# Performance work log

Measured on AMD Instinct MI355X. Metric: run time of the kernel, lower is better.

The kernel has to match this reference:

```python
import jax, jax.numpy as jnp
import numpy as np

H, HD = 8, 64  # num_heads, head_dim
EPS = 1e-6

def rmsnorm(x, scale):
    return x * jax.lax.rsqrt(jnp.mean(x * x, axis=-1, keepdims=True) + EPS) * scale

def lecun(key, shape):
    fan_in = shape[0]
    return jax.random.normal(key, shape, dtype=jnp.float32) * (fan_in ** -0.5)

def setup_inputs() -> dict:
    key = jax.random.key(0)
    ks = jax.random.split(key, 12)
    B, S, D = 2, 512, 512
    hidden = H * HD            # 512
    ffn = 4 * D                # 2048
    return {
        "inputs": jax.random.normal(ks[0], (B, S, D), dtype=jnp.float32),
        "mask": jnp.zeros((B, S), dtype=jnp.float32),
        "carry": jnp.zeros((B, H, HD, HD), dtype=jnp.float32),
        "ln1": jnp.ones((D,), dtype=jnp.float32),
        "Wq": lecun(ks[1], (D, hidden)),
        "Wk": lecun(ks[2], (D, hidden)),
        "Wv": lecun(ks[3], (D, hidden)),
        "attn_ln": jnp.ones((hidden,), dtype=jnp.float32),
        "Wo": lecun(ks[4], (hidden, D)),
        "bo": jnp.zeros((D,), dtype=jnp.float32),
        "ln2": jnp.ones((D,), dtype=jnp.float32),
        "Wg": lecun(ks[5], (D, ffn)),
        "Wu": lecun(ks[6], (D, ffn)),
        "Wd": lecun(ks[7], (ffn, D)),
    }

def reference(inputs, mask, carry, ln1, Wq, Wk, Wv, attn_ln, Wo, bo, ln2, Wg, Wu, Wd):
    B, S, D = inputs.shape
    skip = inputs
    x = rmsnorm(inputs, ln1)
    # projections + relu feature map
    q = jax.nn.relu((x @ Wq).reshape(B, S, H, HD))
    k = jax.nn.relu((x @ Wk).reshape(B, S, H, HD))
    v = (x @ Wv).reshape(B, S, H, HD)
    # matrix-valued state update: Bmat_t = v_t k_t^T  [B,S,H,HD,HD]
    Bmat = v[..., :, None] * k[..., None, :]
    # decay: identity, zeroed where mask==1 (episode reset)
    m = mask[:, :, None, None, None]
    A = jnp.broadcast_to(jnp.eye(HD, dtype=x.dtype), Bmat.shape) * (1.0 - m)

    def binop(lhs, rhs):
        a_i, b_i = lhs
        a_j, b_j = rhs
        return jnp.matmul(a_i, a_j), jnp.matmul(b_i, a_j) + b_j

    cum_decay, hidden_states = jax.lax.associative_scan(binop, (A, Bmat), axis=1)
    # fold in incoming carry
    states = jnp.matmul(carry[:, None], cum_decay) + hidden_states  # [B,S,H,HD,HD]
    attn = jnp.matmul(states, q[..., None]).squeeze(-1).reshape(B, S, H * HD)
    attn = rmsnorm(attn, attn_ln)
    y = attn @ Wo + bo
    final_carry = states[:, -1]
    # residual + SwiGLU FFN
    x = y + skip
    skip2 = x
    x = rmsnorm(x, ln2)
    x = (jax.nn.silu(x @ Wg) * (x @ Wu)) @ Wd
    return (final_carry, x + skip2)
```

## Files before the change

kernel.cpp:

```cpp
#include <hip/hip_runtime.h>
#include <math.h>

typedef __bf16 bf16x8 __attribute__((ext_vector_type(8)));
typedef float  f32x4  __attribute__((ext_vector_type(4)));

constexpr int B_=2, S_=512, D_=512, H_=8, HD_=64, FFN_=2048, NC_=8;
constexpr float EPS_=1e-6f;

__device__ __forceinline__ __bf16 f2bf(float f){
    union{float f;unsigned u;}x; x.f=f;
    unsigned r=(x.u+0x7fffu+((x.u>>16)&1u))>>16;
    union{unsigned short s;__bf16 b;}y; y.s=(unsigned short)r; return y.b;
}
__device__ __forceinline__ float bf2f(unsigned short s){
    union{unsigned u;float f;}x; x.u=((unsigned)s)<<16; return x.f;
}
__device__ __forceinline__ void bf8_f32(uint4 p, float* o){
    unsigned w[4]={p.x,p.y,p.z,p.w};
#pragma unroll
    for(int i=0;i<4;i++){ o[2*i]=bf2f((unsigned short)(w[i]&0xffffu)); o[2*i+1]=bf2f((unsigned short)(w[i]>>16)); }
}
__device__ __forceinline__ f32x4 MF(bf16x8 a, bf16x8 b, f32x4 c){
    return __builtin_amdgcn_mfma_f32_16x16x32_bf16(a,b,c,0,0,0);
}
#define GLOAD16(g,l) __builtin_amdgcn_global_load_lds((__attribute__((address_space(1))) const void*)(g),(__attribute__((address_space(3))) void*)(l),16,0,0)

__device__ __forceinline__ void rowsq_atomic(float* accb, int row0, int lane, float p[4]){
#pragma unroll
    for(int r=0;r<4;r++){
        float v = p[r];
        v += __shfl_xor(v, 1, 64);
        v += __shfl_xor(v, 2, 64);
        v += __shfl_xor(v, 4, 64);
        v += __shfl_xor(v, 8, 64);
        if((lane&15)==0) atomicAdd(accb + row0 + r, v);
    }
}

__global__ __launch_bounds__(256) void prep_k(const float* __restrict__ Wg,
    const float* __restrict__ Wu, const float* __restrict__ Wd,
    const float* __restrict__ Wq, const float* __restrict__ Wk,
    const float* __restrict__ Wv, const float* __restrict__ Wo,
    __bf16* __restrict__ WT, const float* __restrict__ inputs,
    float* __restrict__ rs1, float* __restrict__ rs2acc, float* __restrict__ rs3acc){
    __shared__ __bf16 s[64][72];
    int t = blockIdx.x, tid = threadIdx.x;
    if(t >= 1024){
        int row = (t-1024)*4 + (tid>>6), lane = tid&63;
        const float4* p = (const float4*)(inputs + (size_t)row*D_) + lane*2;
        float4 a=p[0], b=p[1];
        float ss = a.x*a.x+a.y*a.y+a.z*a.z+a.w*a.w + b.x*b.x+b.y*b.y+b.z*b.z+b.w*b.w;
        for(int off=32; off>0; off>>=1) ss += __shfl_down(ss, off, 64);
        if(lane==0) rs1[row] = rsqrtf(ss/(float)D_ + EPS_);
        float4 z = {0.f,0.f,0.f,0.f};
        if(t==1024) ((float4*)rs2acc)[tid] = z;
        if(t==1025) ((float4*)rs3acc)[tid] = z;
        return;
    }
    const float* src; __bf16* dst; int K,N,lt;
    if      (t<256){ src=Wg; dst=WT;          K=512;  N=2048; lt=t; }
    else if (t<512){ src=Wu; dst=WT+1048576;  K=512;  N=2048; lt=t-256; }
    else if (t<768){ src=Wd; dst=WT+2097152;  K=2048; N=512;  lt=t-512; }
    else if (t<832){ src=Wq; dst=WT+3145728;  K=512;  N=512;  lt=t-768; }
    else if (t<896){ src=Wk; dst=WT+3407872;  K=512;  N=512;  lt=t-832; }
    else if (t<960){ src=Wv; dst=WT+3670016;  K=512;  N=512;  lt=t-896; }
    else           { src=Wo; dst=WT+3932160;  K=512;  N=512;  lt=t-960; }
    int nt64 = N>>6, tk = lt/nt64, tn = lt%nt64;
    {
        int jk = tid>>2, jn0 = (tid&3)*16;
        const float* p = src + (size_t)(tk*64+jk)*N + tn*64 + jn0;
        float4 a0=((const float4*)p)[0], a1=((const float4*)p)[1],
               a2=((const float4*)p)[2], a3=((const float4*)p)[3];
        bf16x8 w0, w1;
        w0[0]=f2bf(a0.x); w0[1]=f2bf(a0.y); w0[2]=f2bf(a0.z); w0[3]=f2bf(a0.w);
        w0[4]=f2bf(a1.x); w0[5]=f2bf(a1.y); w0[6]=f2bf(a1.z); w0[7]=f2bf(a1.w);
        w1[0]=f2bf(a2.x); w1[1]=f2bf(a2.y); w1[2]=f2bf(a2.z); w1[3]=f2bf(a2.w);
        w1[4]=f2bf(a3.x); w1[5]=f2bf(a3.y); w1[6]=f2bf(a3.z); w1[7]=f2bf(a3.w);
        *(bf16x8*)&s[jk][jn0] = w0; *(bf16x8*)&s[jk][jn0+8] = w1;
    }
    __syncthreads();
    {
        int jn = tid>>2, jk0 = (tid&3)*16;
        bf16x8 w0, w1;
#pragma unroll
        for(int j=0;j<8;j++){ w0[j]=s[jk0+j][jn]; w1[j]=s[jk0+8+j][jn]; }
        __bf16* q = dst + (size_t)(tn*64+jn)*K + tk*64 + jk0;
        *(bf16x8*)q = w0; *(bf16x8*)(q+8) = w1;
    }
}

__device__ __forceinline__ void stageB2(const __bf16* __restrict__ Bt, int n0, int K, int kk,
                                        __bf16* sB0, __bf16* sB1, int wave, int lane){
    int row = (wave<<4) + (lane>>2), kq = (lane&3)<<3;
    const __bf16* g = Bt + (size_t)(n0+row)*K + kk + kq;
    GLOAD16(g,      sB0 + (wave<<9));
    GLOAD16(g + 32, sB1 + (wave<<9));
    const __bf16* g2 = g + (size_t)64*K;
    GLOAD16(g2,      sB0 + 2048 + (wave<<9));
    GLOAD16(g2 + 32, sB1 + 2048 + (wave<<9));
}
__device__ __forceinline__ void stageB1(const __bf16* __restrict__ Bt, int n0, int K, int kk,
                                        __bf16* sB0, __bf16* sB1, int wave, int lane){
    int row = (wave<<4) + (lane>>2), kq = (lane&3)<<3;
    const __bf16* g = Bt + (size_t)(n0+row)*K + kk + kq;
    GLOAD16(g,      sB0 + (wave<<9));
    GLOAD16(g + 32, sB1 + (wave<<9));
}
__device__ __forceinline__ void stageA_rms_f32(const float* __restrict__ A, const float* __restrict__ rs,
        const float* __restrict__ g, int m0, int K, int kk, __bf16* sA0, __bf16* sA1, int tid){
    int row = tid>>2, kq = (tid&3)<<4;
    float r = rs[m0+row];
    const float4* p = (const float4*)(A + (size_t)(m0+row)*K + kk + kq);
    const float4* gp = (const float4*)(g + kk + kq);
    float4 a[4] = {p[0],p[1],p[2],p[3]};
    float4 gg[4] = {gp[0],gp[1],gp[2],gp[3]};
    bf16x8 w0, w1;
    w0[0]=f2bf(a[0].x*r*gg[0].x); w0[1]=f2bf(a[0].y*r*gg[0].y);
    w0[2]=f2bf(a[0].z*r*gg[0].z); w0[3]=f2bf(a[0].w*r*gg[0].w);
    w0[4]=f2bf(a[1].x*r*gg[1].x); w0[5]=f2bf(a[1].y*r*gg[1].y);
    w0[6]=f2bf(a[1].z*r*gg[1].z); w0[7]=f2bf(a[1].w*r*gg[1].w);
    w1[0]=f2bf(a[2].x*r*gg[2].x); w1[1]=f2bf(a[2].y*r*gg[2].y);
    w1[2]=f2bf(a[2].z*r*gg[2].z); w1[3]=f2bf(a[2].w*r*gg[2].w);
    w1[4]=f2bf(a[3].x*r*gg[3].x); w1[5]=f2bf(a[3].y*r*gg[3].y);
    w1[6]=f2bf(a[3].z*r*gg[3].z); w1[7]=f2bf(a[3].w*r*gg[3].w);
    __bf16* d = (kq<32) ? (sA0 + row*32 + kq) : (sA1 + row*32 + kq-32);
    *(bf16x8*)d = w0; *(bf16x8*)(d+8) = w1;
}
__device__ __forceinline__ void stageA_rms_acc(const __bf16* __restrict__ A, const float* __restrict__ ssq,
        const float* __restrict__ g, int m0, int K, int kk, __bf16* sA0, __bf16* sA1, int tid){
    int row = tid>>2, kq = (tid&3)<<4;
    float r = rsqrtf(ssq[m0+row]*(1.f/(float)D_) + EPS_);
    const __bf16* p = A + (size_t)(m0+row)*K + kk + kq;
    float v[16]; bf8_f32(*(const uint4*)p, v); bf8_f32(*(const uint4*)(p+8), v+8);
    const float4* gp = (const float4*)(g + kk + kq);
    float4 gg[4] = {gp[0],gp[1],gp[2],gp[3]};
    float gf[16] = {gg[0].x,gg[0].y,gg[0].z,gg[0].w, gg[1].x,gg[1].y,gg[1].z,gg[1].w,
                    gg[2].x,gg[2].y,gg[2].z,gg[2].w, gg[3].x,gg[3].y,gg[3].z,gg[3].w};
    bf16x8 w0, w1;
#pragma unroll
    for(int j=0;j<8;j++){ w0[j]=f2bf(v[j]*r*gf[j]); w1[j]=f2bf(v[8+j]*r*gf[8+j]); }
    __bf16* d = (kq<32) ? (sA0 + row*32 + kq) : (sA1 + row*32 + kq-32);
    *(bf16x8*)d = w0; *(bf16x8*)(d+8) = w1;
}
__device__ __forceinline__ void mfma_tile(const __bf16* sA0, const __bf16* sA1,
        const __bf16* sB0, const __bf16* sB1, int wave, int lane, f32x4 acc[4]){
    int ar = (((wave<<4)+(lane&15))<<5) + ((lane>>4)<<3);
    bf16x8 a0 = *(const bf16x8*)(sA0+ar);
    bf16x8 a1 = *(const bf16x8*)(sA1+ar);
#pragma unroll
    for(int nt=0;nt<4;nt++){
        int br = (((nt<<4)+(lane&15))<<5) + ((lane>>4)<<3);
        acc[nt] = MF(a0, *(const bf16x8*)(sB0+br), acc[nt]);
        acc[nt] = MF(a1, *(const bf16x8*)(sB1+br), acc[nt]);
    }
}
__device__ __forceinline__ void mfma_tile8(const __bf16* sA0, const __bf16* sA1,
        const __bf16* sB0, const __bf16* sB1, int wave, int lane, f32x4 acc[8]){
    int ar = (((wave<<4)+(lane&15))<<5) + ((lane>>4)<<3);
    bf16x8 a0 = *(const bf16x8*)(sA0+ar);
    bf16x8 a1 = *(const bf16x8*)(sA1+ar);
#pragma unroll
    for(int nt=0;nt<8;nt++){
        int br = (((nt<<4)+(lane&15))<<5) + ((lane>>4)<<3);
        acc[nt] = MF(a0, *(const bf16x8*)(sB0+br), acc[nt]);
        acc[nt] = MF(a1, *(const bf16x8*)(sB1+br), acc[nt]);
    }
}

__global__ __launch_bounds__(256) void gemm_qkv_k(const float* __restrict__ in,
        const float* __restrict__ rs1, const float* __restrict__ ln1,
        const __bf16* __restrict__ Bt, __bf16* __restrict__ Qb,
        __bf16* __restrict__ Kb, __bf16* __restrict__ Vb){
    __shared__ __bf16 sA0[2048], sA1[2048], sB0[4096], sB1[4096];
    int tid=threadIdx.x, wave=tid>>6, lane=tid&63;
    int n0 = blockIdx.x*128, m0 = blockIdx.y*64;
    f32x4 acc[8] = {};
    for(int kk=0; kk<512; kk+=64){
        stageB2(Bt, n0, 512, kk, sB0, sB1, wave, lane);
        stageA_rms_f32(in, rs1, ln1, m0, 512, kk, sA0, sA1, tid);
        __syncthreads();
        mfma_tile8(sA0,sA1,sB0,sB1,wave,lane,acc);
        __syncthreads();
    }
    int seg = n0>>9, nc = n0&511;
    __bf16* Out = seg==0 ? Qb : (seg==1 ? Kb : Vb);
    bool rl = seg<2;
    int r0 = (wave<<4) + ((lane>>4)<<2);
#pragma unroll
    for(int nt=0;nt<8;nt++){
        int col = nc + nt*16 + (lane&15);
#pragma unroll
        for(int r=0;r<4;r++){
            float v = acc[nt][r]; if(rl) v = fmaxf(v,0.f);
            Out[(size_t)(m0+r0+r)*512 + col] = f2bf(v);
        }
    }
}

__global__ __launch_bounds__(256) void scanA_k(const __bf16* __restrict__ Kb,
        const __bf16* __restrict__ Vb, const float* __restrict__ mask,
        __bf16* __restrict__ MS, float* __restrict__ Pws){
    int bid = blockIdx.x;
    int c = bid&7, h = (bid>>3)&7, b = bid>>6;
    __shared__ __bf16 sKT0[2048], sKT1[2048], sVT0[2048], sVT1[2048];
    __shared__ float scv[64], ssp[64];
    int tid = threadIdx.x, wave = tid>>6, lane = tid&63;
    const __bf16* Kg = Kb + (size_t)(b*512 + c*64)*512 + h*64;
    const __bf16* Vg = Vb + (size_t)(b*512 + c*64)*512 + h*64;
    if(tid<64) scv[tid] = 1.f - mask[b*512 + c*64 + tid];
    __syncthreads();
    if(tid==0){
        float sp = 1.f;
        for(int t=63;t>=0;--t){ ssp[t]=sp; sp*=scv[t]; }
        Pws[bid] = sp;
    }
    __syncthreads();
#pragma unroll
    for(int p=0;p<2;p++){
        int t = (tid>>3) + p*32, i0 = (tid&7)*8;
        uint4 kr = *(const uint4*)(Kg + (size_t)t*512 + i0);
        uint4 vr = *(const uint4*)(Vg + (size_t)t*512 + i0);
        const __bf16* kp = (const __bf16*)&kr;
        const unsigned short* vp = (const unsigned short*)&vr;
        float sp = ssp[t];
        __bf16* kh = p ? sKT1 : sKT0;
        __bf16* vh = p ? sVT1 : sVT0;
#pragma unroll
        for(int j=0;j<8;j++){
            kh[(i0+j)*32 + (t&31)] = kp[j];
            vh[(i0+j)*32 + (t&31)] = f2bf(bf2f(vp[j])*sp);
        }
    }
    __syncthreads();
    f32x4 am[4] = {};
    mfma_tile(sVT0, sVT1, sKT0, sKT1, wave, lane, am);
    __bf16* Mo = MS + (size_t)bid*4096;
    int r0 = (wave<<4) + ((lane>>4)<<2);
#pragma unroll
    for(int nt=0;nt<4;nt++){
        int j = nt*16 + (lane&15);
#pragma unroll
        for(int r=0;r<4;r++) Mo[(size_t)(r0+r)*64 + j] = f2bf(am[nt][r]);
    }
}

__global__ __launch_bounds__(256) void scanC_k(const __bf16* __restrict__ Qb,
        const __bf16* __restrict__ Kb, const __bf16* __restrict__ Vb,
        const float* __restrict__ mask, const __bf16* __restrict__ MS,
        const float* __restrict__ carry, const float* __restrict__ Pws,
        float* __restrict__ carry_out, __bf16* __restrict__ attn,
        float* __restrict__ rs2acc){
    int bid = blockIdx.x;
    int c = bid&7, h = (bid>>3)&7, b = bid>>6;
    int bh = b*H_ + h;
    __shared__ __bf16 sQ0[2048], sQ1[2048], sK0[2048], sK1[2048];
    __shared__ __bf16 sS0[2048], sS1[2048];
    __shared__ __bf16 sVT0[2048], sVT1[2048];
    __shared__ __bf16 sW0[2048], sW1[2048];
    __shared__ float Wtab[64][64];
    __shared__ float scv[64], pp[64];
    int tid = threadIdx.x, wave = tid>>6, lane = tid&63;
    const __bf16* Qg = Qb + (size_t)(b*512 + c*64)*512 + h*64;
    const __bf16* Kg = Kb + (size_t)(b*512 + c*64)*512 + h*64;
    const __bf16* Vg = Vb + (size_t)(b*512 + c*64)*512 + h*64;

    stageB1(Qg, 0, 512, 0, sQ0, sQ1, wave, lane);
    stageB1(Kg, 0, 512, 0, sK0, sK1, wave, lane);
    if(tid<64) scv[tid] = 1.f - mask[b*512 + c*64 + tid];
#pragma unroll
    for(int p=0;p<2;p++){
        int u = (tid>>3) + p*32, i0 = (tid&7)*8;
        uint4 vr = *(const uint4*)(Vg + (size_t)u*512 + i0);
        const __bf16* vp = (const __bf16*)&vr;
        __bf16* vh = p ? sVT1 : sVT0;
#pragma unroll
        for(int j=0;j<8;j++) vh[(i0+j)*32 + (u&31)] = vp[j];
    }
    {
        int i = tid>>2, j0 = (tid&3)*16;
        float s[16];
        const float* ci = carry + (size_t)bh*4096 + i*64 + j0;
        const float4* c4 = (const float4*)ci;
        float4 s4[4] = {c4[0],c4[1],c4[2],c4[3]};
        float* sp = (float*)s4;
#pragma unroll
        for(int j=0;j<16;j++) s[j]=sp[j];
        for(int cc=0; cc<c; ++cc){
            float P = Pws[bh*8+cc];
            const __bf16* mp = MS + ((size_t)bh*8+cc)*4096 + i*64 + j0;
            float mv[16]; bf8_f32(*(const uint4*)mp, mv); bf8_f32(*(const uint4*)(mp+8), mv+8);
#pragma unroll
            for(int j=0;j<16;j++) s[j] = s[j]*P + mv[j];
        }
        bf16x8 w0, w1;
#pragma unroll
        for(int j=0;j<8;j++){ w0[j]=f2bf(s[j]); w1[j]=f2bf(s[8+j]); }
        __bf16* d = (j0<32) ? (sS0 + i*32 + j0) : (sS1 + i*32 + j0-32);
        *(bf16x8*)d = w0; *(bf16x8*)(d+8) = w1;
        if(c==7){
            float P = Pws[bh*8+7];
            const __bf16* mp = MS + ((size_t)bh*8+7)*4096 + i*64 + j0;
            float mv[16]; bf8_f32(*(const uint4*)mp, mv); bf8_f32(*(const uint4*)(mp+8), mv+8);
            float4 o4[4];
            float* ov = (float*)o4;
#pragma unroll
            for(int j=0;j<16;j++) ov[j] = s[j]*P + mv[j];
            float4* co = (float4*)(carry_out + (size_t)bh*4096 + i*64 + j0);
            co[0]=o4[0]; co[1]=o4[1]; co[2]=o4[2]; co[3]=o4[3];
        }
    }
    __syncthreads();
    if(tid<64){
        int u = tid; float w = 1.f;
        for(int t=0;t<64;t++){
            if(t>u) w *= scv[t];
            Wtab[u][t] = (t<u) ? 0.f : w;
        }
    }
    if(tid==64){
        float p=1.f;
        for(int t=0;t<64;t++){ p*=scv[t]; pp[t]=p; }
    }
    f32x4 sc[4] = {};
    mfma_tile(sK0, sK1, sQ0, sQ1, wave, lane, sc);
    __syncthreads();
    {
        int u0 = (wave<<4) + ((lane>>4)<<2);
#pragma unroll
        for(int nt=0;nt<4;nt++){
            int t = nt*16 + (lane&15);
#pragma unroll
            for(int r=0;r<4;r++){
                int u = u0 + r;
                float v = sc[nt][r] * Wtab[u][t];
                ((u<32) ? sW0 : sW1)[t*32 + (u&31)] = f2bf(v);
            }
        }
    }
    __syncthreads();
    f32x4 aI[4] = {}, aX[4] = {};
    mfma_tile(sW0, sW1, sVT0, sVT1, wave, lane, aI);
    mfma_tile(sQ0, sQ1, sS0, sS1, wave, lane, aX);
    int t0 = (wave<<4) + ((lane>>4)<<2);
    float psum[4] = {0.f,0.f,0.f,0.f};
#pragma unroll
    for(int nt=0;nt<4;nt++){
        int i = nt*16 + (lane&15);
#pragma unroll
        for(int r=0;r<4;r++){
            int t = t0 + r;
            float o = aI[nt][r] + aX[nt][r]*pp[t];
            attn[(size_t)(b*512 + c*64 + t)*512 + h*64 + i] = f2bf(o);
            psum[r] += o*o;
        }
    }
    rowsq_atomic(rs2acc, b*512 + c*64 + t0, lane, psum);
}

__global__ __launch_bounds__(256) void gemm_wo_k(const __bf16* __restrict__ attn,
        const float* __restrict__ rs2acc, const float* __restrict__ aln,
        const __bf16* __restrict__ Bt, const float* __restrict__ bo,
        const float* __restrict__ skip, float* __restrict__ outx,
        __bf16* __restrict__ X1, float* __restrict__ rs3acc){
    __shared__ __bf16 sA0[2048], sA1[2048], sB0[4096], sB1[4096];
    int tid=threadIdx.x, wave=tid>>6, lane=tid&63;
    int n0 = blockIdx.x*128, m0 = blockIdx.y*64;
    f32x4 acc[8] = {};
    for(int kk=0; kk<512; kk+=64){
        stageB2(Bt, n0, 512, kk, sB0, sB1, wave, lane);
        stageA_rms_acc(attn, rs2acc, aln, m0, 512, kk, sA0, sA1, tid);
        __syncthreads();
        mfma_tile8(sA0,sA1,sB0,sB1,wave,lane,acc);
        __syncthreads();
    }
    int r0 = (wave<<4) + ((lane>>4)<<2);
    float psum[4] = {0.f,0.f,0.f,0.f};
#pragma unroll
    for(int nt=0;nt<8;nt++){
        int col = n0 + nt*16 + (lane&15);
#pragma unroll
        for(int r=0;r<4;r++){
            int row = m0+r0+r;
            float v = acc[nt][r] + bo[col] + skip[(size_t)row*512+col];
            outx[(size_t)row*512+col] = v;
            X1[(size_t)row*512+col] = f2bf(v);
            psum[r] += v*v;
        }
    }
    rowsq_atomic(rs3acc, m0+r0, lane, psum);
}

__global__ __launch_bounds__(256) void gemm_dual_k(const __bf16* __restrict__ X1,
        const float* __restrict__ rs3acc, const float* __restrict__ ln2,
        const __bf16* __restrict__ Gt, const __bf16* __restrict__ Ut,
        __bf16* __restrict__ Hb){
    __shared__ __bf16 sA0[2048], sA1[2048], sG0[4096], sG1[4096], sU0[4096], sU1[4096];
    int tid=threadIdx.x, wave=tid>>6, lane=tid&63;
    int n0 = blockIdx.x*128, m0 = blockIdx.y*64;
    f32x4 ag[8] = {}, au[8] = {};
    for(int kk=0; kk<512; kk+=64){
        stageB2(Gt, n0, 512, kk, sG0, sG1, wave, lane);
        stageB2(Ut, n0, 512, kk, sU0, sU1, wave, lane);
        stageA_rms_acc(X1, rs3acc, ln2, m0, 512, kk, sA0, sA1, tid);
        __syncthreads();
        {
            int ar = (((wave<<4)+(lane&15))<<5) + ((lane>>4)<<3);
            bf16x8 a0 = *(const bf16x8*)(sA0+ar);
            bf16x8 a1 = *(const bf16x8*)(sA1+ar);
#pragma unroll
            for(int nt=0;nt<8;nt++){
                int br = (((nt<<4)+(lane&15))<<5) + ((lane>>4)<<3);
                ag[nt] = MF(a0, *(const bf16x8*)(sG0+br), ag[nt]);
                ag[nt] = MF(a1, *(const bf16x8*)(sG1+br), ag[nt]);
                au[nt] = MF(a0, *(const bf16x8*)(sU0+br), au[nt]);
                au[nt] = MF(a1, *(const bf16x8*)(sU1+br), au[nt]);
            }
        }
        __syncthreads();
    }
    int r0 = (wave<<4) + ((lane>>4)<<2);
#pragma unroll
    for(int nt=0;nt<8;nt++){
        int col = n0 + nt*16 + (lane&15);
#pragma unroll
        for(int r=0;r<4;r++){
            float gv = ag[nt][r], uv = au[nt][r];
            float hv = (gv / (1.f + __expf(-gv))) * uv;
            Hb[(size_t)(m0+r0+r)*FFN_ + col] = f2bf(hv);
        }
    }
}

__global__ __launch_bounds__(256) void gemm_wd_k(const __bf16* __restrict__ Hb,
        const __bf16* __restrict__ Bt, float* __restrict__ outx){
    __shared__ __bf16 sA0[2048], sA1[2048], sB0[4096], sB1[4096];
    int tid=threadIdx.x, wave=tid>>6, lane=tid&63;
    int n0 = blockIdx.x*128, m0 = blockIdx.y*64, ks = blockIdx.z*512;
    f32x4 acc[8] = {};
    int row = (wave<<4) + (lane>>2), kq = (lane&3)<<3;
    for(int kk=ks; kk<ks+512; kk+=64){
        stageB2(Bt, n0, FFN_, kk, sB0, sB1, wave, lane);
        const __bf16* g = Hb + (size_t)(m0+row)*FFN_ + kk + kq;
        GLOAD16(g,      sA0 + (wave<<9));
        GLOAD16(g + 32, sA1 + (wave<<9));
        __syncthreads();
        mfma_tile8(sA0,sA1,sB0,sB1,wave,lane,acc);
        __syncthreads();
    }
    int r0 = (wave<<4) + ((lane>>4)<<2);
#pragma unroll
    for(int nt=0;nt<8;nt++){
        int col = n0 + nt*16 + (lane&15);
#pragma unroll
        for(int r=0;r<4;r++)
            atomicAdd(&outx[(size_t)(m0+r0+r)*512 + col], acc[nt][r]);
    }
}

extern "C" void kernel_launch(void* const* d_in, const int* in_sizes, int n_in,
                              void* d_out, int out_size, void* d_ws, size_t ws_size,
                              hipStream_t stream) {
    const float* inputs  = (const float*)d_in[0];
    const float* mask    = (const float*)d_in[1];
    const float* carry   = (const float*)d_in[2];
    const float* ln1     = (const float*)d_in[3];
    const float* Wq      = (const float*)d_in[4];
    const float* Wk      = (const float*)d_in[5];
    const float* Wv      = (const float*)d_in[6];
    const float* attn_ln = (const float*)d_in[7];
    const float* Wo      = (const float*)d_in[8];
    const float* bo      = (const float*)d_in[9];
    const float* ln2     = (const float*)d_in[10];
    const float* Wg      = (const float*)d_in[11];
    const float* Wu      = (const float*)d_in[12];
    const float* Wd      = (const float*)d_in[13];

    float* out_carry = (float*)d_out;
    float* out_x     = (float*)d_out + 65536;

    __bf16* wb = (__bf16*)d_ws;
    float*  wf = (float*)d_ws;
    __bf16* WgT   = wb;
    __bf16* WuT   = wb + 1048576;
    __bf16* WdT   = wb + 2097152;
    __bf16* WqkvT = wb + 3145728;
    __bf16* WoT   = wb + 3932160;
    __bf16* Qb    = wb + 4194304;
    __bf16* Kb    = wb + 4718592;
    __bf16* Vb    = wb + 5242880;
    __bf16* Hb    = wb + 3145728;
    __bf16* MS    = wb + 5767168;
    float*  Pws   = wf + 3145728;
    float*  rs1   = wf + 3145856;
    float*  rs2a  = wf + 3146880;
    float*  rs3a  = wf + 3147904;

    prep_k<<<dim3(1280), dim3(256), 0, stream>>>(Wg,Wu,Wd,Wq,Wk,Wv,Wo, wb, inputs, rs1, rs2a, rs3a);
    gemm_qkv_k<<<dim3(12,16), dim3(256), 0, stream>>>(inputs, rs1, ln1, WqkvT, Qb, Kb, Vb);
    scanA_k<<<dim3(128), dim3(256), 0, stream>>>(Kb, Vb, mask, MS, Pws);
    scanC_k<<<dim3(128), dim3(256), 0, stream>>>(Qb, Kb, Vb, mask, MS, carry, Pws, out_carry, Qb, rs2a);
    gemm_wo_k<<<dim3(4,16), dim3(256), 0, stream>>>(Qb, rs2a, attn_ln, WoT, bo, inputs, out_x, Vb, rs3a);
    gemm_dual_k<<<dim3(16,16), dim3(256), 0, stream>>>(Vb, rs3a, ln2, WgT, WuT, Hb);
    gemm_wd_k<<<dim3(4,16,4), dim3(256), 0, stream>>>(Hb, WdT, out_x);
}
```

Measured before the change: 169.9 us.

## Double-buffer GEMM shared tiles and halve N-tile to raise block count

All four GEMM kernels (qkv, wo, dual gate/up, wd) switch to double-buffered LDS. The next K-slice's global loads are issued before the MFMA on the current slice, and one barrier per iteration replaces two. The N tile shrinks from 128 to 64, so the grids double and more workgroups run on the many CUs. The RMS scale is now loaded once per kernel instead of per K-step, and the prep transpose's read mapping is changed to reduce LDS bank conflicts. Smaller tiles mean less B-reuse and more A reloads.

```diff
diff --git a/kernel.cpp b/kernel.cpp
--- a/kernel.cpp
+++ b/kernel.cpp
@@ -80,25 +80,15 @@
     }
     __syncthreads();
     {
-        int jn = tid>>2, jk0 = (tid&3)*16;
+        int jn = tid&63, jkq = (tid>>6)*16;
         bf16x8 w0, w1;
 #pragma unroll
-        for(int j=0;j<8;j++){ w0[j]=s[jk0+j][jn]; w1[j]=s[jk0+8+j][jn]; }
-        __bf16* q = dst + (size_t)(tn*64+jn)*K + tk*64 + jk0;
+        for(int j=0;j<8;j++){ w0[j]=s[jkq+j][jn]; w1[j]=s[jkq+8+j][jn]; }
+        __bf16* q = dst + (size_t)(tn*64+jn)*K + tk*64 + jkq;
         *(bf16x8*)q = w0; *(bf16x8*)(q+8) = w1;
     }
 }
 
-__device__ __forceinline__ void stageB2(const __bf16* __restrict__ Bt, int n0, int K, int kk,
-                                        __bf16* sB0, __bf16* sB1, int wave, int lane){
-    int row = (wave<<4) + (lane>>2), kq = (lane&3)<<3;
-    const __bf16* g = Bt + (size_t)(n0+row)*K + kk + kq;
-    GLOAD16(g,      sB0 + (wave<<9));
-    GLOAD16(g + 32, sB1 + (wave<<9));
-    const __bf16* g2 = g + (size_t)64*K;
-    GLOAD16(g2,      sB0 + 2048 + (wave<<9));
-    GLOAD16(g2 + 32, sB1 + 2048 + (wave<<9));
-}
 __device__ __forceinline__ void stageB1(const __bf16* __restrict__ Bt, int n0, int K, int kk,
                                         __bf16* sB0, __bf16* sB1, int wave, int lane){
     int row = (wave<<4) + (lane>>2), kq = (lane&3)<<3;
@@ -106,36 +96,47 @@
     GLOAD16(g,      sB0 + (wave<<9));
     GLOAD16(g + 32, sB1 + (wave<<9));
 }
-__device__ __forceinline__ void stageA_rms_f32(const float* __restrict__ A, const float* __restrict__ rs,
-        const float* __restrict__ g, int m0, int K, int kk, __bf16* sA0, __bf16* sA1, int tid){
+struct ARf { float4 a0,a1,a2,a3, g0,g1,g2,g3; };
+__device__ __forceinline__ ARf loadA_f32(const float* __restrict__ A, const float* __restrict__ g,
+                                         int m0, int K, int kk, int tid){
     int row = tid>>2, kq = (tid&3)<<4;
-    float r = rs[m0+row];
     const float4* p = (const float4*)(A + (size_t)(m0+row)*K + kk + kq);
     const float4* gp = (const float4*)(g + kk + kq);
-    float4 a[4] = {p[0],p[1],p[2],p[3]};
-    float4 gg[4] = {gp[0],gp[1],gp[2],gp[3]};
+    ARf o;
+    o.a0=p[0]; o.a1=p[1]; o.a2=p[2]; o.a3=p[3];
+    o.g0=gp[0]; o.g1=gp[1]; o.g2=gp[2]; o.g3=gp[3];
+    return o;
+}
+__device__ __forceinline__ void writeA_f32(const ARf& o, float r, __bf16* sA0, __bf16* sA1, int tid){
+    int row = tid>>2, kq = (tid&3)<<4;
     bf16x8 w0, w1;
-    w0[0]=f2bf(a[0].x*r*gg[0].x); w0[1]=f2bf(a[0].y*r*gg[0].y);
-    w0[2]=f2bf(a[0].z*r*gg[0].z); w0[3]=f2bf(a[0].w*r*gg[0].w);
-    w0[4]=f2bf(a[1].x*r*gg[1].x); w0[5]=f2bf(a[1].y*r*gg[1].y);
-    w0[6]=f2bf(a[1].z*r*gg[1].z); w0[7]=f2bf(a[1].w*r*gg[1].w);
-    w1[0]=f2bf(a[2].x*r*gg[2].x); w1[1]=f2bf(a[2].y*r*gg[2].y);
-    w1[2]=f2bf(a[2].z*r*gg[2].z); w1[3]=f2bf(a[2].w*r*gg[2].w);
-    w1[4]=f2bf(a[3].x*r*gg[3].x); w1[5]=f2bf(a[3].y*r*gg[3].y);
-    w1[6]=f2bf(a[3].z*r*gg[3].z); w1[7]=f2bf(a[3].w*r*gg[3].w);
+    w0[0]=f2bf(o.a0.x*r*o.g0.x); w0[1]=f2bf(o.a0.y*r*o.g0.y);
+    w0[2]=f2bf(o.a0.z*r*o.g0.z); w0[3]=f2bf(o.a0.w*r*o.g0.w);
+    w0[4]=f2bf(o.a1.x*r*o.g1.x); w0[5]=f2bf(o.a1.y*r*o.g1.y);
+    w0[6]=f2bf(o.a1.z*r*o.g1.z); w0[7]=f2bf(o.a1.w*r*o.g1.w);
+    w1[0]=f2bf(o.a2.x*r*o.g2.x); w1[1]=f2bf(o.a2.y*r*o.g2.y);
+    w1[2]=f2bf(o.a2.z*r*o.g2.z); w1[3]=f2bf(o.a2.w*r*o.g2.w);
+    w1[4]=f2bf(o.a3.x*r*o.g3.x); w1[5]=f2bf(o.a3.y*r*o.g3.y);
+    w1[6]=f2bf(o.a3.z*r*o.g3.z); w1[7]=f2bf(o.a3.w*r*o.g3.w);
     __bf16* d = (kq<32) ? (sA0 + row*32 + kq) : (sA1 + row*32 + kq-32);
     *(bf16x8*)d = w0; *(bf16x8*)(d+8) = w1;
 }
-__device__ __forceinline__ void stageA_rms_acc(const __bf16* __restrict__ A, const float* __restrict__ ssq,
-        const float* __restrict__ g, int m0, int K, int kk, __bf16* sA0, __bf16* sA1, int tid){
+struct ARb { uint4 p0,p1; float4 g0,g1,g2,g3; };
+__device__ __forceinline__ ARb loadA_bf16(const __bf16* __restrict__ A, const float* __restrict__ g,
+                                          int m0, int K, int kk, int tid){
     int row = tid>>2, kq = (tid&3)<<4;
-    float r = rsqrtf(ssq[m0+row]*(1.f/(float)D_) + EPS_);
     const __bf16* p = A + (size_t)(m0+row)*K + kk + kq;
-    float v[16]; bf8_f32(*(const uint4*)p, v); bf8_f32(*(const uint4*)(p+8), v+8);
     const float4* gp = (const float4*)(g + kk + kq);
-    float4 gg[4] = {gp[0],gp[1],gp[2],gp[3]};
-    float gf[16] = {gg[0].x,gg[0].y,gg[0].z,gg[0].w, gg[1].x,gg[1].y,gg[1].z,gg[1].w,
-                    gg[2].x,gg[2].y,gg[2].z,gg[2].w, gg[3].x,gg[3].y,gg[3].z,gg[3].w};
+    ARb o;
+    o.p0 = *(const uint4*)p; o.p1 = *(const uint4*)(p+8);
+    o.g0=gp[0]; o.g1=gp[1]; o.g2=gp[2]; o.g3=gp[3];
+    return o;
+}
+__device__ __forceinline__ void writeA_bf16(const ARb& o, float r, __bf16* sA0, __bf16* sA1, int tid){
+    int row = tid>>2, kq = (tid&3)<<4;
+    float v[16]; bf8_f32(o.p0, v); bf8_f32(o.p1, v+8);
+    float gf[16] = {o.g0.x,o.g0.y,o.g0.z,o.g0.w, o.g1.x,o.g1.y,o.g1.z,o.g1.w,
+                    o.g2.x,o.g2.y,o.g2.z,o.g2.w, o.g3.x,o.g3.y,o.g3.z,o.g3.w};
     bf16x8 w0, w1;
 #pragma unroll
     for(int j=0;j<8;j++){ w0[j]=f2bf(v[j]*r*gf[j]); w1[j]=f2bf(v[8+j]*r*gf[8+j]); }
@@ -154,45 +155,47 @@
         acc[nt] = MF(a1, *(const bf16x8*)(sB1+br), acc[nt]);
     }
 }
-__device__ __forceinline__ void mfma_tile8(const __bf16* sA0, const __bf16* sA1,
-        const __bf16* sB0, const __bf16* sB1, int wave, int lane, f32x4 acc[8]){
-    int ar = (((wave<<4)+(lane&15))<<5) + ((lane>>4)<<3);
-    bf16x8 a0 = *(const bf16x8*)(sA0+ar);
-    bf16x8 a1 = *(const bf16x8*)(sA1+ar);
-#pragma unroll
-    for(int nt=0;nt<8;nt++){
-        int br = (((nt<<4)+(lane&15))<<5) + ((lane>>4)<<3);
-        acc[nt] = MF(a0, *(const bf16x8*)(sB0+br), acc[nt]);
-        acc[nt] = MF(a1, *(const bf16x8*)(sB1+br), acc[nt]);
-    }
-}
 
 __global__ __launch_bounds__(256) void gemm_qkv_k(const float* __restrict__ in,
         const float* __restrict__ rs1, const float* __restrict__ ln1,
         const __bf16* __restrict__ Bt, __bf16* __restrict__ Qb,
         __bf16* __restrict__ Kb, __bf16* __restrict__ Vb){
-    __shared__ __bf16 sA0[2048], sA1[2048], sB0[4096], sB1[4096];
+    __shared__ __bf16 sA0[2][2048], sA1[2][2048], sB0[2][2048], sB1[2][2048];
     int tid=threadIdx.x, wave=tid>>6, lane=tid&63;
-    int n0 = blockIdx.x*128, m0 = blockIdx.y*64;
-    f32x4 acc[8] = {};
-    for(int kk=0; kk<512; kk+=64){
-        stageB2(Bt, n0, 512, kk, sB0, sB1, wave, lane);
-        stageA_rms_f32(in, rs1, ln1, m0, 512, kk, sA0, sA1, tid);
-        __syncthreads();
-        mfma_tile8(sA0,sA1,sB0,sB1,wave,lane,acc);
-        __syncthreads();
+    int n0 = blockIdx.x*64, m0 = blockIdx.y*64;
+    float r = rs1[m0+(tid>>2)];
+    f32x4 acc[4] = {};
+    {
+        ARf a = loadA_f32(in, ln1, m0, 512, 0, tid);
+        stageB1(Bt, n0, 512, 0, sB0[0], sB1[0], wave, lane);
+        writeA_f32(a, r, sA0[0], sA1[0], tid);
+        __syncthreads();
+    }
+    int cur = 0;
+#pragma unroll
+    for(int it=0; it<8; ++it){
+        int nxt = cur^1;
+        ARf a;
+        if(it<7){
+            a = loadA_f32(in, ln1, m0, 512, (it+1)*64, tid);
+            stageB1(Bt, n0, 512, (it+1)*64, sB0[nxt], sB1[nxt], wave, lane);
+        }
+        mfma_tile(sA0[cur],sA1[cur],sB0[cur],sB1[cur],wave,lane,acc);
+        if(it<7) writeA_f32(a, r, sA0[nxt], sA1[nxt], tid);
+        __syncthreads();
+        cur = nxt;
     }
     int seg = n0>>9, nc = n0&511;
     __bf16* Out = seg==0 ? Qb : (seg==1 ? Kb : Vb);
     bool rl = seg<2;
     int r0 = (wave<<4) + ((lane>>4)<<2);
 #pragma unroll
-    for(int nt=0;nt<8;nt++){
+    for(int nt=0;nt<4;nt++){
         int col = nc + nt*16 + (lane&15);
 #pragma unroll
-        for(int r=0;r<4;r++){
-            float v = acc[nt][r]; if(rl) v = fmaxf(v,0.f);
-            Out[(size_t)(m0+r0+r)*512 + col] = f2bf(v);
+        for(int rr=0;rr<4;rr++){
+            float v = acc[nt][rr]; if(rl) v = fmaxf(v,0.f);
+            Out[(size_t)(m0+r0+rr)*512 + col] = f2bf(v);
         }
     }
 }
@@ -279,8 +282,7 @@
     {
         int i = tid>>2, j0 = (tid&3)*16;
         float s[16];
-        const float* ci = carry + (size_t)bh*4096 + i*64 + j0;
-        const float4* c4 = (const float4*)ci;
+        const float4* c4 = (const float4*)(carry + (size_t)bh*4096 + i*64 + j0);
         float4 s4[4] = {c4[0],c4[1],c4[2],c4[3]};
         float* sp = (float*)s4;
 #pragma unroll
@@ -362,29 +364,43 @@
         const __bf16* __restrict__ Bt, const float* __restrict__ bo,
         const float* __restrict__ skip, float* __restrict__ outx,
         __bf16* __restrict__ X1, float* __restrict__ rs3acc){
-    __shared__ __bf16 sA0[2048], sA1[2048], sB0[4096], sB1[4096];
+    __shared__ __bf16 sA0[2][2048], sA1[2][2048], sB0[2][2048], sB1[2][2048];
     int tid=threadIdx.x, wave=tid>>6, lane=tid&63;
-    int n0 = blockIdx.x*128, m0 = blockIdx.y*64;
-    f32x4 acc[8] = {};
-    for(int kk=0; kk<512; kk+=64){
-        stageB2(Bt, n0, 512, kk, sB0, sB1, wave, lane);
-        stageA_rms_acc(attn, rs2acc, aln, m0, 512, kk, sA0, sA1, tid);
-        __syncthreads();
-        mfma_tile8(sA0,sA1,sB0,sB1,wave,lane,acc);
-        __syncthreads();
+    int n0 = blockIdx.x*64, m0 = blockIdx.y*64;
+    float r = rsqrtf(rs2acc[m0+(tid>>2)]*(1.f/(float)D_) + EPS_);
+    f32x4 acc[4] = {};
+    {
+        ARb a = loadA_bf16(attn, aln, m0, 512, 0, tid);
+        stageB1(Bt, n0, 512, 0, sB0[0], sB1[0], wave, lane);
+        writeA_bf16(a, r, sA0[0], sA1[0], tid);
+        __syncthreads();
+    }
+    int cur = 0;
+#pragma unroll
+    for(int it=0; it<8; ++it){
+        int nxt = cur^1;
+        ARb a;
+        if(it<7){
+            a = loadA_bf16(attn, aln, m0, 512, (it+1)*64, tid);
+            stageB1(Bt, n0, 512, (it+1)*64, sB0[nxt], sB1[nxt], wave, lane);
+        }
+        mfma_tile(sA0[cur],sA1[cur],sB0[cur],sB1[cur],wave,lane,acc);
+        if(it<7) writeA_bf16(a, r, sA0[nxt], sA1[nxt], tid);
+        __syncthreads();
+        cur = nxt;
     }
     int r0 = (wave<<4) + ((lane>>4)<<2);
     float psum[4] = {0.f,0.f,0.f,0.f};
 #pragma unroll
-    for(int nt=0;nt<8;nt++){
+    for(int nt=0;nt<4;nt++){
         int col = n0 + nt*16 + (lane&15);
 #pragma unroll
-        for(int r=0;r<4;r++){
-            int row = m0+r0+r;
-            float v = acc[nt][r] + bo[col] + skip[(size_t)row*512+col];
+        for(int rr=0;rr<4;rr++){
+            int row = m0+r0+rr;
+            float v = acc[nt][rr] + bo[col] + skip[(size_t)row*512+col];
             outx[(size_t)row*512+col] = v;
             X1[(size_t)row*512+col] = f2bf(v);
-            psum[r] += v*v;
+            psum[rr] += v*v;
         }
     }
     rowsq_atomic(rs3acc, m0+r0, lane, psum);
@@ -394,62 +410,91 @@
         const float* __restrict__ rs3acc, const float* __restrict__ ln2,
         const __bf16* __restrict__ Gt, const __bf16* __restrict__ Ut,
         __bf16* __restrict__ Hb){
-    __shared__ __bf16 sA0[2048], sA1[2048], sG0[4096], sG1[4096], sU0[4096], sU1[4096];
+    __shared__ __bf16 sA0[2][2048], sA1[2][2048];
+    __shared__ __bf16 sG0[2][2048], sG1[2][2048], sU0[2][2048], sU1[2][2048];
     int tid=threadIdx.x, wave=tid>>6, lane=tid&63;
-    int n0 = blockIdx.x*128, m0 = blockIdx.y*64;
-    f32x4 ag[8] = {}, au[8] = {};
-    for(int kk=0; kk<512; kk+=64){
-        stageB2(Gt, n0, 512, kk, sG0, sG1, wave, lane);
-        stageB2(Ut, n0, 512, kk, sU0, sU1, wave, lane);
-        stageA_rms_acc(X1, rs3acc, ln2, m0, 512, kk, sA0, sA1, tid);
-        __syncthreads();
+    int n0 = blockIdx.x*64, m0 = blockIdx.y*64;
+    float r = rsqrtf(rs3acc[m0+(tid>>2)]*(1.f/(float)D_) + EPS_);
+    f32x4 ag[4] = {}, au[4] = {};
+    {
+        ARb a = loadA_bf16(X1, ln2, m0, 512, 0, tid);
+        stageB1(Gt, n0, 512, 0, sG0[0], sG1[0], wave, lane);
+        stageB1(Ut, n0, 512, 0, sU0[0], sU1[0], wave, lane);
+        writeA_bf16(a, r, sA0[0], sA1[0], tid);
+        __syncthreads();
+    }
+    int cur = 0;
+#pragma unroll
+    for(int it=0; it<8; ++it){
+        int nxt = cur^1;
+        ARb a;
+        if(it<7){
+            a = loadA_bf16(X1, ln2, m0, 512, (it+1)*64, tid);
+            stageB1(Gt, n0, 512, (it+1)*64, sG0[nxt], sG1[nxt], wave, lane);
+            stageB1(Ut, n0, 512, (it+1)*64, sU0[nxt], sU1[nxt], wave, lane);
+        }
         {
             int ar = (((wave<<4)+(lane&15))<<5) + ((lane>>4)<<3);
-            bf16x8 a0 = *(const bf16x8*)(sA0+ar);
-            bf16x8 a1 = *(const bf16x8*)(sA1+ar);
-#pragma unroll
-            for(int nt=0;nt<8;nt++){
+            bf16x8 a0 = *(const bf16x8*)(sA0[cur]+ar);
+            bf16x8 a1 = *(const bf16x8*)(sA1[cur]+ar);
+#pragma unroll
+            for(int nt=0;nt<4;nt++){
                 int br = (((nt<<4)+(lane&15))<<5) + ((lane>>4)<<3);
-                ag[nt] = MF(a0, *(const bf16x8*)(sG0+br), ag[nt]);
-                ag[nt] = MF(a1, *(const bf16x8*)(sG1+br), ag[nt]);
-                au[nt] = MF(a0, *(const bf16x8*)(sU0+br), au[nt]);
-                au[nt] = MF(a1, *(const bf16x8*)(sU1+br), au[nt]);
+                ag[nt] = MF(a0, *(const bf16x8*)(sG0[cur]+br), ag[nt]);
+                ag[nt] = MF(a1, *(const bf16x8*)(sG1[cur]+br), ag[nt]);
+                au[nt] = MF(a0, *(const bf16x8*)(sU0[cur]+br), au[nt]);
+                au[nt] = MF(a1, *(const bf16x8*)(sU1[cur]+br), au[nt]);
             }
         }
-        __syncthreads();
+        if(it<7) writeA_bf16(a, r, sA0[nxt], sA1[nxt], tid);
+        __syncthreads();
+        cur = nxt;
     }
     int r0 = (wave<<4) + ((lane>>4)<<2);
 #pragma unroll
-    for(int nt=0;nt<8;nt++){
+    for(int nt=0;nt<4;nt++){
         int col = n0 + nt*16 + (lane&15);
 #pragma unroll
-        for(int r=0;r<4;r++){
-            float gv = ag[nt][r], uv = au[nt][r];
+        for(int rr=0;rr<4;rr++){
+            float gv = ag[nt][rr], uv = au[nt][rr];
             float hv = (gv / (1.f + __expf(-gv))) * uv;
-            Hb[(size_t)(m0+r0+r)*FFN_ + col] = f2bf(hv);
+            Hb[(size_t)(m0+r0+rr)*FFN_ + col] = f2bf(hv);
         }
     }
 }
 
 __global__ __launch_bounds__(256) void gemm_wd_k(const __bf16* __restrict__ Hb,
         const __bf16* __restrict__ Bt, float* __restrict__ outx){
-    __shared__ __bf16 sA0[2048], sA1[2048], sB0[4096], sB1[4096];
+    __shared__ __bf16 sA0[2][2048], sA1[2][2048], sB0[2][2048], sB1[2][2048];
     int tid=threadIdx.x, wave=tid>>6, lane=tid&63;
-    int n0 = blockIdx.x*128, m0 = blockIdx.y*64, ks = blockIdx.z*512;
-    f32x4 acc[8] = {};
+    int n0 = blockIdx.x*64, m0 = blockIdx.y*64, ks = blockIdx.z*512;
+    f32x4 acc[4] = {};
     int row = (wave<<4) + (lane>>2), kq = (lane&3)<<3;
-    for(int kk=ks; kk<ks+512; kk+=64){
-        stageB2(Bt, n0, FFN_, kk, sB0, sB1, wave, lane);
-        const __bf16* g = Hb + (size_t)(m0+row)*FFN_ + kk + kq;
-        GLOAD16(g,      sA0 + (wave<<9));
-        GLOAD16(g + 32, sA1 + (wave<<9));
-        __syncthreads();
-        mfma_tile8(sA0,sA1,sB0,sB1,wave,lane,acc);
-        __syncthreads();
+    {
+        stageB1(Bt, n0, FFN_, ks, sB0[0], sB1[0], wave, lane);
+        const __bf16* g = Hb + (size_t)(m0+row)*FFN_ + ks + kq;
+        GLOAD16(g,      sA0[0] + (wave<<9));
+        GLOAD16(g + 32, sA1[0] + (wave<<9));
+        __syncthreads();
+    }
+    int cur = 0;
+#pragma unroll
+    for(int it=0; it<8; ++it){
+        int nxt = cur^1;
+        if(it<7){
+            int kk = ks + (it+1)*64;
+            stageB1(Bt, n0, FFN_, kk, sB0[nxt], sB1[nxt], wave, lane);
+            const __bf16* g = Hb + (size_t)(m0+row)*FFN_ + kk + kq;
+            GLOAD16(g,      sA0[nxt] + (wave<<9));
+            GLOAD16(g + 32, sA1[nxt] + (wave<<9));
+        }
+        mfma_tile(sA0[cur],sA1[cur],sB0[cur],sB1[cur],wave,lane,acc);
+        __syncthreads();
+        cur = nxt;
     }
     int r0 = (wave<<4) + ((lane>>4)<<2);
 #pragma unroll
-    for(int nt=0;nt<8;nt++){
+    for(int nt=0;nt<4;nt++){
         int col = n0 + nt*16 + (lane&15);
 #pragma unroll
         for(int r=0;r<4;r++)
@@ -496,10 +541,10 @@
     float*  rs3a  = wf + 3147904;
 
     prep_k<<<dim3(1280), dim3(256), 0, stream>>>(Wg,Wu,Wd,Wq,Wk,Wv,Wo, wb, inputs, rs1, rs2a, rs3a);
-    gemm_qkv_k<<<dim3(12,16), dim3(256), 0, stream>>>(inputs, rs1, ln1, WqkvT, Qb, Kb, Vb);
+    gemm_qkv_k<<<dim3(24,16), dim3(256), 0, stream>>>(inputs, rs1, ln1, WqkvT, Qb, Kb, Vb);
     scanA_k<<<dim3(128), dim3(256), 0, stream>>>(Kb, Vb, mask, MS, Pws);
     scanC_k<<<dim3(128), dim3(256), 0, stream>>>(Qb, Kb, Vb, mask, MS, carry, Pws, out_carry, Qb, rs2a);
-    gemm_wo_k<<<dim3(4,16), dim3(256), 0, stream>>>(Qb, rs2a, attn_ln, WoT, bo, inputs, out_x, Vb, rs3a);
-    gemm_dual_k<<<dim3(16,16), dim3(256), 0, stream>>>(Vb, rs3a, ln2, WgT, WuT, Hb);
-    gemm_wd_k<<<dim3(4,16,4), dim3(256), 0, stream>>>(Hb, WdT, out_x);
-}
+    gemm_wo_k<<<dim3(8,16), dim3(256), 0, stream>>>(Qb, rs2a, attn_ln, WoT, bo, inputs, out_x, Vb, rs3a);
+    gemm_dual_k<<<dim3(32,16), dim3(256), 0, stream>>>(Vb, rs3a, ln2, WgT, WuT, Hb);
+    gemm_wd_k<<<dim3(8,16,4), dim3(256), 0, stream>>>(Hb, WdT, out_x);
+}
```

Result: faster. 161.7 us (-4.9%).
